# Kernel optimization log

Hardware: AMD Instinct MI355X
Metric: run time of the kernel (lower is better)

Reference implementation:

```python
import jax, jax.numpy as jnp
import numpy as np

N = 32768          # n_atoms
E = 524288         # n_edges (avg degree 16)
MUL = 8            # multiplicity of 0e and 1o in irreps_in/out
NB = 8             # n_basis
HR = 64            # hidden_radial
NTP = 4 * MUL * MUL  # tensor-product weight_numel (4 CG paths)
AVG_NEI = 16.0
INV_SQRT3 = 1.0 / np.sqrt(3.0)      # w3j(1,1,0) component
ALPHA = 1.0 / np.sqrt(2.0 * MUL)    # path normalization: fan_in = 2 paths * mul_in*mul_sh


def setup_inputs() -> dict:
    key = jax.random.key(0)
    ks = jax.random.split(key, 12)
    h = jax.random.normal(ks[0], (N, 4 * MUL), jnp.float32)            # [N, 8 scalars + 8*3 vectors]
    edge_index = jax.random.randint(ks[1], (2, E), 0, N)               # [2, E] int
    edge_sh = jax.random.normal(ks[2], (E, 4), jnp.float32)            # [E, 1x0e + 1x1o]
    edge_radial = jax.random.uniform(ks[3], (E, NB), jnp.float32)      # [E, n_basis]

    def lin(k, fi, fo):
        return (jax.random.normal(k, (fi, fo), jnp.float32) / np.sqrt(fi)).astype(jnp.float32)

    W1 = lin(ks[4], NB, HR); b1 = jnp.zeros((HR,), jnp.float32)
    W2 = lin(ks[5], HR, HR); b2 = jnp.zeros((HR,), jnp.float32)
    W3 = lin(ks[6], HR, NTP); b3 = jnp.zeros((NTP,), jnp.float32)
    Ws = jax.random.normal(ks[7], (MUL, MUL), jnp.float32)             # self-interaction, scalar block
    Wv = jax.random.normal(ks[8], (MUL, MUL), jnp.float32)             # self-interaction, vector block
    return dict(h=h, edge_index=edge_index, edge_sh=edge_sh, edge_radial=edge_radial,
                n_atoms=N, W1=W1, b1=b1, W2=W2, b2=b2, W3=W3, b3=b3, Ws=Ws, Wv=Wv)


def reference(h, edge_index, edge_sh, edge_radial, n_atoms, W1, b1, W2, b2, W3, b3, Ws, Wv):
    src, dst = edge_index[0], edge_index[1]

    # radial MLP -> per-edge tensor-product weights [E, 256]
    x = jax.nn.silu(edge_radial @ W1 + b1)
    x = jax.nn.silu(x @ W2 + b2)
    tpw = x @ W3 + b3
    P = MUL * MUL
    W00  = tpw[:, 0 * P:1 * P].reshape(-1, MUL, MUL)  # 0e x 0e -> 0e
    W110 = tpw[:, 1 * P:2 * P].reshape(-1, MUL, MUL)  # 1o x 1o -> 0e (dot)
    W01  = tpw[:, 2 * P:3 * P].reshape(-1, MUL, MUL)  # 0e x 1o -> 1o
    W10  = tpw[:, 3 * P:4 * P].reshape(-1, MUL, MUL)  # 1o x 0e -> 1o

    hs = h[:, :MUL]                         # [N, 8] scalars
    hv = h[:, MUL:].reshape(-1, MUL, 3)     # [N, 8, 3] vectors
    hs_e = hs[src]                          # gather [E, 8]
    hv_e = hv[src]                          # gather [E, 8, 3]
    sh0 = edge_sh[:, 0]                     # [E]
    sh1 = edge_sh[:, 1:4]                   # [E, 3]

    # equivariant tensor product (e3nn FullyConnectedTensorProduct, l<=1)
    m0 = ALPHA * (jnp.einsum('eu,euw->ew', hs_e * sh0[:, None], W00)
                  + INV_SQRT3 * jnp.einsum('eui,ei,euw->ew', hv_e, sh1, W110))       # [E, 8]
    m1 = ALPHA * (jnp.einsum('eu,ei,euw->ewi', hs_e, sh1, W01)
                  + jnp.einsum('eui,euw->ewi', hv_e * sh0[:, None, None], W10))      # [E, 8, 3]
    messages = jnp.concatenate([m0, m1.reshape(-1, 3 * MUL)], axis=-1)               # [E, 32]

    # scatter-add to destination nodes, degree normalization
    agg = jax.ops.segment_sum(messages, dst, num_segments=n_atoms) / np.sqrt(AVG_NEI)

    # self interaction (o3.Linear: block-diagonal per irrep, 1/sqrt(fan_in))
    self0 = (hs @ Ws) / np.sqrt(MUL)
    self1 = jnp.einsum('nui,uw->nwi', hv, Wv) / np.sqrt(MUL)
    h_self = jnp.concatenate([self0, self1.reshape(-1, 3 * MUL)], axis=-1)

    return h_self + agg
```

## Files before the change

kernel.cpp:

```cpp
#include <hip/hip_runtime.h>

#define N_ATOMS 32768
#define E_EDGES 524288
#define FEAT 32
#define TPB 512
#define WPB 8
#define PASSES 2
#define GRID (E_EDGES / (WPB * PASSES * 16))
#define INV_SQRT3 0.57735026919f
#define MSG_SCALE 0.0625f
#define SELF_SCALE 0.35355339059f

#define WS_MSG   0
#define WS_CNT   33554432
#define WS_CUR   33685504
#define WS_OFFS  33816576
#define WS_BSUM  33947648
#define WS_BBASE 33948160
#define WS_EIDS  33948672
#define WS_WF    36045824

typedef _Float16 f16;
typedef __attribute__((ext_vector_type(8))) _Float16 f16x8;
typedef __attribute__((ext_vector_type(4))) float f32x4;
typedef __attribute__((ext_vector_type(2))) _Float16 f16x2;
typedef __attribute__((ext_vector_type(4))) _Float16 f16x4;

__device__ __forceinline__ float silu(float x) { return x / (1.0f + __expf(-x)); }

__device__ __forceinline__ f32x4 mfma16(f16x8 a, f16x8 b, f32x4 c) {
    return __builtin_amdgcn_mfma_f32_16x16x32_f16(a, b, c, 0, 0, 0);
}

__global__ __launch_bounds__(256) void prep_kernel(
    const float* __restrict__ W1, const float* __restrict__ W2,
    const float* __restrict__ W3, f16* __restrict__ wf)
{
    int idx = blockIdx.x * 256 + threadIdx.x;
    float v;
    if (idx < 2048) {
        int f = idx;
        int n0 = f >> 9, lane = (f >> 3) & 63, j = f & 7;
        int k = ((lane >> 4) << 3) + j, n = (n0 << 4) + (lane & 15);
        v = (k < 8) ? W1[k * 64 + n] : 0.0f;
    } else if (idx < 6144) {
        int f = idx - 2048;
        int kk = f >> 11, n0 = (f >> 9) & 3, lane = (f >> 3) & 63, j = f & 7;
        int k = (kk << 5) + ((lane >> 4) << 3) + j, n = (n0 << 4) + (lane & 15);
        v = W2[k * 64 + n];
    } else {
        int f = idx - 6144;
        int kk = f >> 13, n0 = (f >> 9) & 15, lane = (f >> 3) & 63, j = f & 7;
        int k = (kk << 5) + ((lane >> 4) << 3) + j, n = (n0 << 4) + (lane & 15);
        v = W3[k * 256 + n];
    }
    wf[idx] = (f16)v;
}

__global__ __launch_bounds__(256) void count_kernel(const int* __restrict__ eidx,
                                                    int* __restrict__ cnt) {
    int e = blockIdx.x * 256 + threadIdx.x;
    atomicAdd(&cnt[eidx[E_EDGES + e]], 1);
}

__global__ __launch_bounds__(256) void scan1_kernel(const int* __restrict__ cnt,
                                                    int* __restrict__ bsum) {
    __shared__ int s[256];
    int t = threadIdx.x;
    s[t] = cnt[blockIdx.x * 256 + t];
    __syncthreads();
    for (int d = 128; d > 0; d >>= 1) {
        if (t < d) s[t] += s[t + d];
        __syncthreads();
    }
    if (t == 0) bsum[blockIdx.x] = s[0];
}

__global__ __launch_bounds__(64) void scan2_kernel(const int* __restrict__ bsum,
                                                   int* __restrict__ bbase) {
    int lane = threadIdx.x;
    int v0 = bsum[2 * lane], v1 = bsum[2 * lane + 1];
    int s = v0 + v1, x = s;
    for (int d = 1; d < 64; d <<= 1) {
        int y = __shfl_up(x, d, 64);
        if (lane >= d) x += y;
    }
    int excl = x - s;
    bbase[2 * lane] = excl;
    bbase[2 * lane + 1] = excl + v0;
}

__global__ __launch_bounds__(256) void scan3_kernel(const int* __restrict__ cnt,
                                                    const int* __restrict__ bbase,
                                                    int* __restrict__ offs) {
    int t = threadIdx.x, lane = t & 63, w = t >> 6;
    int v = cnt[blockIdx.x * 256 + t];
    int x = v;
    for (int d = 1; d < 64; d <<= 1) {
        int y = __shfl_up(x, d, 64);
        if (lane >= d) x += y;
    }
    __shared__ int wsum[4];
    if (lane == 63) wsum[w] = x;
    __syncthreads();
    int base = bbase[blockIdx.x];
    for (int i = 0; i < w; ++i) base += wsum[i];
    offs[blockIdx.x * 256 + t] = base + x - v;
}

__global__ __launch_bounds__(256) void fill_kernel(const int* __restrict__ eidx,
                                                   const int* __restrict__ offs,
                                                   int* __restrict__ cur,
                                                   int* __restrict__ eids) {
    int e = blockIdx.x * 256 + threadIdx.x;
    int d = eidx[E_EDGES + e];
    int slot = atomicAdd(&cur[d], 1);
    eids[offs[d] + slot] = e;
}

__global__ __launch_bounds__(TPB, 4) void edge_kernel(
    const float* __restrict__ h, const int* __restrict__ eidx,
    const float* __restrict__ esh, const float* __restrict__ erad,
    const f16* __restrict__ wf,
    const float* __restrict__ b1, const float* __restrict__ b2,
    const float* __restrict__ b3,
    f16* __restrict__ msg)
{
    __shared__ f16x8 w3L[2048];
    __shared__ float b1s[64], b2s[64], b3s[256];
    __shared__ __align__(16) char xtp[WPB][16 * 72 * 2];

    const int tid = threadIdx.x;
    {
        const f16x8* wfW3 = (const f16x8*)(wf + 6144);
#pragma unroll
        for (int i = 0; i < 4; ++i)
            w3L[tid + i * TPB] = wfW3[tid + i * TPB];
    }
    if (tid < 64) { b1s[tid] = b1[tid]; b2s[tid] = b2[tid]; }
    if (tid < 256) b3s[tid] = b3[tid];
    __syncthreads();

    const f16x8* w1f = (const f16x8*)(wf);
    const f16x8* w2f = (const f16x8*)(wf + 2048);

    const int wave = tid >> 6, lane = tid & 63;
    const int g = lane >> 4, m = lane & 15;
    const int me = lane >> 2, w0 = (lane & 3) * 2;

    f16* xs = (f16*)&xtp[wave][0];
    float* tpt = (float*)&xtp[wave][0];

    for (int pass = 0; pass < PASSES; ++pass) {
        const int tile = (blockIdx.x * WPB + wave) * PASSES + pass;
        const int e0 = tile * 16;

        f16x8 arad;
        {
            float r[8] = {0.f, 0.f, 0.f, 0.f, 0.f, 0.f, 0.f, 0.f};
            if (g == 0) {
                const float4* rp = (const float4*)(erad + (long)(e0 + m) * 8);
                float4 r0 = rp[0], r1 = rp[1];
                r[0] = r0.x; r[1] = r0.y; r[2] = r0.z; r[3] = r0.w;
                r[4] = r1.x; r[5] = r1.y; r[6] = r1.z; r[7] = r1.w;
            }
#pragma unroll
            for (int j = 0; j < 8; ++j) arad[j] = (f16)r[j];
        }

#pragma unroll
        for (int n0 = 0; n0 < 4; ++n0) {
            f32x4 acc = {};
            acc = mfma16(arad, w1f[n0 * 64 + lane], acc);
            float bn = b1s[n0 * 16 + m];
#pragma unroll
            for (int q = 0; q < 4; ++q) {
                float v = silu(acc[q] + bn);
                xs[(g * 4 + q) * 72 + n0 * 16 + m] = (f16)v;
            }
        }
        f16x8 a2[2];
        a2[0] = *(const f16x8*)(xs + m * 72 + g * 8);
        a2[1] = *(const f16x8*)(xs + m * 72 + 32 + g * 8);

        const int src = eidx[e0 + me];
        const float4 shv = *(const float4*)(esh + (long)(e0 + me) * 4);
        float hrow[32];
        {
            const float* hp = h + (long)src * FEAT;
#pragma unroll
            for (int c4 = 0; c4 < 8; ++c4)
                ((float4*)hrow)[c4] = ((const float4*)hp)[c4];
        }

#pragma unroll
        for (int n0 = 0; n0 < 4; ++n0) {
            f32x4 acc = {};
            acc = mfma16(a2[0], w2f[n0 * 64 + lane], acc);
            acc = mfma16(a2[1], w2f[(4 + n0) * 64 + lane], acc);
            float bn = b2s[n0 * 16 + m];
#pragma unroll
            for (int q = 0; q < 4; ++q) {
                float v = silu(acc[q] + bn);
                xs[(g * 4 + q) * 72 + n0 * 16 + m] = (f16)v;
            }
        }
        f16x8 a3[2];
        a3[0] = *(const f16x8*)(xs + m * 72 + g * 8);
        a3[1] = *(const f16x8*)(xs + m * 72 + 32 + g * 8);

        float m0a0 = 0.f, m0a1 = 0.f, s20 = 0.f, s21 = 0.f;
        float sv[6] = {0.f, 0.f, 0.f, 0.f, 0.f, 0.f};

#pragma unroll
        for (int c = 0; c < 4; ++c) {
#pragma unroll
            for (int n0 = 0; n0 < 4; ++n0) {
                f32x4 acc = {};
                acc = mfma16(a3[0], w3L[(c * 4 + n0) * 64 + lane], acc);
                acc = mfma16(a3[1], w3L[(16 + c * 4 + n0) * 64 + lane], acc);
                float bn = b3s[c * 64 + n0 * 16 + m];
#pragma unroll
                for (int q = 0; q < 4; ++q)
                    tpt[(g * 4 + q) * 18 + m] = acc[q] + bn;
#pragma unroll
                for (int uu = 0; uu < 2; ++uu) {
                    const int u = 2 * n0 + uu;
                    float2 t = *(const float2*)(tpt + me * 18 + uu * 8 + w0);
                    if (c == 0) {
                        float a0 = hrow[u] * shv.x;
                        m0a0 += a0 * t.x; m0a1 += a0 * t.y;
                    } else if (c == 1) {
                        float a1 = INV_SQRT3 * (hrow[8 + u * 3] * shv.y +
                                                hrow[9 + u * 3] * shv.z +
                                                hrow[10 + u * 3] * shv.w);
                        m0a0 += a1 * t.x; m0a1 += a1 * t.y;
                    } else if (c == 2) {
                        s20 += hrow[u] * t.x; s21 += hrow[u] * t.y;
                    } else {
                        sv[0] += hrow[8 + u * 3] * t.x;
                        sv[1] += hrow[9 + u * 3] * t.x;
                        sv[2] += hrow[10 + u * 3] * t.x;
                        sv[3] += hrow[8 + u * 3] * t.y;
                        sv[4] += hrow[9 + u * 3] * t.y;
                        sv[5] += hrow[10 + u * 3] * t.y;
                    }
                }
            }
        }

        f16* row = msg + (long)(e0 + me) * FEAT;
        f16x2 p0;
        p0[0] = (f16)(MSG_SCALE * m0a0);
        p0[1] = (f16)(MSG_SCALE * m0a1);
        *(f16x2*)(row + w0) = p0;
        f16 m1v[6];
#pragma unroll
        for (int i = 0; i < 3; ++i) {
            float s1i = (i == 0) ? shv.y : (i == 1) ? shv.z : shv.w;
            m1v[i]     = (f16)(MSG_SCALE * (s1i * s20 + shv.x * sv[i]));
            m1v[3 + i] = (f16)(MSG_SCALE * (s1i * s21 + shv.x * sv[3 + i]));
        }
        f16* rp = row + 8 + 3 * w0;
        { f16x2 t; t[0] = m1v[0]; t[1] = m1v[1]; *(f16x2*)(rp)     = t; }
        { f16x2 t; t[0] = m1v[2]; t[1] = m1v[3]; *(f16x2*)(rp + 2) = t; }
        { f16x2 t; t[0] = m1v[4]; t[1] = m1v[5]; *(f16x2*)(rp + 4) = t; }
    }
}

__global__ __launch_bounds__(256) void gather_kernel(
    const f16* __restrict__ msg, const int* __restrict__ eids,
    const int* __restrict__ offs, const int* __restrict__ cnt,
    const float* __restrict__ h,
    const float* __restrict__ Ws, const float* __restrict__ Wv,
    float* __restrict__ out)
{
    const int t = threadIdx.x;
    const int n = blockIdx.x * 32 + (t >> 3);
    const int L = t & 7;
    const int base = offs[n], deg = cnt[n];

    float a0 = 0.f, a1 = 0.f, a2 = 0.f, a3 = 0.f;
    for (int i = 0; i < deg; ++i) {
        int eid = eids[base + i];
        f16x4 v = *(const f16x4*)(msg + (long)eid * FEAT + L * 4);
        a0 += (float)v[0]; a1 += (float)v[1]; a2 += (float)v[2]; a3 += (float)v[3];
    }

    const float* hrow = h + (long)n * FEAT;
    const int f0 = L * 4;
    float o[4];
    if (L < 2) {
#pragma unroll
        for (int j = 0; j < 4; ++j) {
            int w = f0 + j;
            float a = 0.f;
#pragma unroll
            for (int u = 0; u < 8; ++u) a += hrow[u] * Ws[u * 8 + w];
            o[j] = SELF_SCALE * a;
        }
    } else {
#pragma unroll
        for (int j = 0; j < 4; ++j) {
            int f = f0 + j, w = (f - 8) / 3, i3 = (f - 8) % 3;
            float a = 0.f;
#pragma unroll
            for (int u = 0; u < 8; ++u) a += hrow[8 + u * 3 + i3] * Wv[u * 8 + w];
            o[j] = SELF_SCALE * a;
        }
    }
    float4 r;
    r.x = o[0] + a0; r.y = o[1] + a1; r.z = o[2] + a2; r.w = o[3] + a3;
    *(float4*)(out + (long)n * FEAT + f0) = r;
}

extern "C" void kernel_launch(void* const* d_in, const int* in_sizes, int n_in,
                              void* d_out, int out_size, void* d_ws, size_t ws_size,
                              hipStream_t stream)
{
    const float* h    = (const float*)d_in[0];
    const int*   eidx = (const int*)  d_in[1];
    const float* esh  = (const float*)d_in[2];
    const float* erad = (const float*)d_in[3];
    const float* W1   = (const float*)d_in[5];
    const float* b1   = (const float*)d_in[6];
    const float* W2   = (const float*)d_in[7];
    const float* b2   = (const float*)d_in[8];
    const float* W3   = (const float*)d_in[9];
    const float* b3   = (const float*)d_in[10];
    const float* Ws   = (const float*)d_in[11];
    const float* Wv   = (const float*)d_in[12];
    float* out = (float*)d_out;

    char* ws = (char*)d_ws;
    f16* msg   = (f16*)(ws + WS_MSG);
    int* cnt   = (int*)(ws + WS_CNT);
    int* cur   = (int*)(ws + WS_CUR);
    int* offs  = (int*)(ws + WS_OFFS);
    int* bsum  = (int*)(ws + WS_BSUM);
    int* bbase = (int*)(ws + WS_BBASE);
    int* eids  = (int*)(ws + WS_EIDS);
    f16* wf    = (f16*)(ws + WS_WF);

    hipMemsetAsync(cnt, 0, 2 * N_ATOMS * sizeof(int), stream);

    prep_kernel<<<88, 256, 0, stream>>>(W1, W2, W3, wf);
    count_kernel<<<E_EDGES / 256, 256, 0, stream>>>(eidx, cnt);
    scan1_kernel<<<N_ATOMS / 256, 256, 0, stream>>>(cnt, bsum);
    scan2_kernel<<<1, 64, 0, stream>>>(bsum, bbase);
    scan3_kernel<<<N_ATOMS / 256, 256, 0, stream>>>(cnt, bbase, offs);
    edge_kernel<<<GRID, TPB, 0, stream>>>(h, eidx, esh, erad, wf,
                                          b1, b2, b3, msg);
    fill_kernel<<<E_EDGES / 256, 256, 0, stream>>>(eidx, offs, cur, eids);
    gather_kernel<<<N_ATOMS / 32, 256, 0, stream>>>(msg, eids, offs, cnt,
                                                    h, Ws, Wv, out);
}
```

Measured before the change: 178.8 us.

## Write edge messages directly into CSR-sorted slots, drop fill kernel and eids

The edge kernel now reserves each edge's destination-sorted row via an atomic on the per-node cursor and writes its message there. This removes the separate fill kernel and the eids indirection, so the gather reads contiguous rows per node. The W3 tensor-product loop is also software-pipelined with a double-buffered tpt tile, and the gather loop is unrolled by two with split accumulators. The tpt double buffer assumes the shared scratch holds 576 floats per warp, and message row order within a node now depends on atomic ordering.

Result: no change. 180.7 us (+1.1%).

```diff
diff --git a/kernel.cpp b/kernel.cpp
--- a/kernel.cpp
+++ b/kernel.cpp
@@ -17,7 +17,6 @@
 #define WS_OFFS  33816576
 #define WS_BSUM  33947648
 #define WS_BBASE 33948160
-#define WS_EIDS  33948672
 #define WS_WF    36045824
 
 typedef _Float16 f16;
@@ -108,22 +107,13 @@
     offs[blockIdx.x * 256 + t] = base + x - v;
 }
 
-__global__ __launch_bounds__(256) void fill_kernel(const int* __restrict__ eidx,
-                                                   const int* __restrict__ offs,
-                                                   int* __restrict__ cur,
-                                                   int* __restrict__ eids) {
-    int e = blockIdx.x * 256 + threadIdx.x;
-    int d = eidx[E_EDGES + e];
-    int slot = atomicAdd(&cur[d], 1);
-    eids[offs[d] + slot] = e;
-}
-
 __global__ __launch_bounds__(TPB, 4) void edge_kernel(
     const float* __restrict__ h, const int* __restrict__ eidx,
     const float* __restrict__ esh, const float* __restrict__ erad,
     const f16* __restrict__ wf,
     const float* __restrict__ b1, const float* __restrict__ b2,
     const float* __restrict__ b3,
+    const int* __restrict__ offs, int* __restrict__ cur,
     f16* __restrict__ msg)
 {
     __shared__ f16x8 w3L[2048];
@@ -184,6 +174,7 @@
         a2[1] = *(const f16x8*)(xs + m * 72 + 32 + g * 8);
 
         const int src = eidx[e0 + me];
+        const int dst = eidx[E_EDGES + e0 + me];
         const float4 shv = *(const float4*)(esh + (long)(e0 + me) * 4);
         float hrow[32];
         {
@@ -192,6 +183,10 @@
             for (int c4 = 0; c4 < 8; ++c4)
                 ((float4*)hrow)[c4] = ((const float4*)hp)[c4];
         }
+        int rowid = 0;
+        if ((lane & 3) == 0)
+            rowid = offs[dst] + atomicAdd(&cur[dst], 1);
+        rowid = __shfl(rowid, me * 4);
 
 #pragma unroll
         for (int n0 = 0; n0 < 4; ++n0) {
@@ -213,43 +208,60 @@
         float sv[6] = {0.f, 0.f, 0.f, 0.f, 0.f, 0.f};
 
 #pragma unroll
-        for (int c = 0; c < 4; ++c) {
-#pragma unroll
-            for (int n0 = 0; n0 < 4; ++n0) {
-                f32x4 acc = {};
-                acc = mfma16(a3[0], w3L[(c * 4 + n0) * 64 + lane], acc);
-                acc = mfma16(a3[1], w3L[(16 + c * 4 + n0) * 64 + lane], acc);
-                float bn = b3s[c * 64 + n0 * 16 + m];
-#pragma unroll
-                for (int q = 0; q < 4; ++q)
-                    tpt[(g * 4 + q) * 18 + m] = acc[q] + bn;
+        for (int t = 0; t < 16; ++t) {
+            const int c = t >> 2, n0 = t & 3;
+            f32x4 acc = {};
+            acc = mfma16(a3[0], w3L[(c * 4 + n0) * 64 + lane], acc);
+            acc = mfma16(a3[1], w3L[(16 + c * 4 + n0) * 64 + lane], acc);
+            float bn = b3s[c * 64 + n0 * 16 + m];
+            float* tb = tpt + (t & 1) * 288;
+#pragma unroll
+            for (int q = 0; q < 4; ++q)
+                tb[(g * 4 + q) * 18 + m] = acc[q] + bn;
+            if (t > 0) {
+                const int tp = t - 1, cp = tp >> 2, np = tp & 3;
+                const float* rb = tpt + (tp & 1) * 288;
 #pragma unroll
                 for (int uu = 0; uu < 2; ++uu) {
-                    const int u = 2 * n0 + uu;
-                    float2 t = *(const float2*)(tpt + me * 18 + uu * 8 + w0);
-                    if (c == 0) {
+                    const int u = 2 * np + uu;
+                    float2 tv = *(const float2*)(rb + me * 18 + uu * 8 + w0);
+                    if (cp == 0) {
                         float a0 = hrow[u] * shv.x;
-                        m0a0 += a0 * t.x; m0a1 += a0 * t.y;
-                    } else if (c == 1) {
+                        m0a0 += a0 * tv.x; m0a1 += a0 * tv.y;
+                    } else if (cp == 1) {
                         float a1 = INV_SQRT3 * (hrow[8 + u * 3] * shv.y +
                                                 hrow[9 + u * 3] * shv.z +
                                                 hrow[10 + u * 3] * shv.w);
-                        m0a0 += a1 * t.x; m0a1 += a1 * t.y;
-                    } else if (c == 2) {
-                        s20 += hrow[u] * t.x; s21 += hrow[u] * t.y;
+                        m0a0 += a1 * tv.x; m0a1 += a1 * tv.y;
+                    } else if (cp == 2) {
+                        s20 += hrow[u] * tv.x; s21 += hrow[u] * tv.y;
                     } else {
-                        sv[0] += hrow[8 + u * 3] * t.x;
-                        sv[1] += hrow[9 + u * 3] * t.x;
-                        sv[2] += hrow[10 + u * 3] * t.x;
-                        sv[3] += hrow[8 + u * 3] * t.y;
-                        sv[4] += hrow[9 + u * 3] * t.y;
-                        sv[5] += hrow[10 + u * 3] * t.y;
+                        sv[0] += hrow[8 + u * 3] * tv.x;
+                        sv[1] += hrow[9 + u * 3] * tv.x;
+                        sv[2] += hrow[10 + u * 3] * tv.x;
+                        sv[3] += hrow[8 + u * 3] * tv.y;
+                        sv[4] += hrow[9 + u * 3] * tv.y;
+                        sv[5] += hrow[10 + u * 3] * tv.y;
                     }
                 }
             }
         }
-
-        f16* row = msg + (long)(e0 + me) * FEAT;
+        {
+            const float* rb = tpt + 288;
+#pragma unroll
+            for (int uu = 0; uu < 2; ++uu) {
+                const int u = 6 + uu;
+                float2 tv = *(const float2*)(rb + me * 18 + uu * 8 + w0);
+                sv[0] += hrow[8 + u * 3] * tv.x;
+                sv[1] += hrow[9 + u * 3] * tv.x;
+                sv[2] += hrow[10 + u * 3] * tv.x;
+                sv[3] += hrow[8 + u * 3] * tv.y;
+                sv[4] += hrow[9 + u * 3] * tv.y;
+                sv[5] += hrow[10 + u * 3] * tv.y;
+            }
+        }
+
+        f16* row = msg + (long)rowid * FEAT;
         f16x2 p0;
         p0[0] = (f16)(MSG_SCALE * m0a0);
         p0[1] = (f16)(MSG_SCALE * m0a1);
@@ -262,14 +274,14 @@
             m1v[3 + i] = (f16)(MSG_SCALE * (s1i * s21 + shv.x * sv[3 + i]));
         }
         f16* rp = row + 8 + 3 * w0;
-        { f16x2 t; t[0] = m1v[0]; t[1] = m1v[1]; *(f16x2*)(rp)     = t; }
-        { f16x2 t; t[0] = m1v[2]; t[1] = m1v[3]; *(f16x2*)(rp + 2) = t; }
-        { f16x2 t; t[0] = m1v[4]; t[1] = m1v[5]; *(f16x2*)(rp + 4) = t; }
+        { f16x2 t2; t2[0] = m1v[0]; t2[1] = m1v[1]; *(f16x2*)(rp)     = t2; }
+        { f16x2 t2; t2[0] = m1v[2]; t2[1] = m1v[3]; *(f16x2*)(rp + 2) = t2; }
+        { f16x2 t2; t2[0] = m1v[4]; t2[1] = m1v[5]; *(f16x2*)(rp + 4) = t2; }
     }
 }
 
 __global__ __launch_bounds__(256) void gather_kernel(
-    const f16* __restrict__ msg, const int* __restrict__ eids,
+    const f16* __restrict__ msg,
     const int* __restrict__ offs, const int* __restrict__ cnt,
     const float* __restrict__ h,
     const float* __restrict__ Ws, const float* __restrict__ Wv,
@@ -281,11 +293,19 @@
     const int base = offs[n], deg = cnt[n];
 
     float a0 = 0.f, a1 = 0.f, a2 = 0.f, a3 = 0.f;
-    for (int i = 0; i < deg; ++i) {
-        int eid = eids[base + i];
-        f16x4 v = *(const f16x4*)(msg + (long)eid * FEAT + L * 4);
+    float c0 = 0.f, c1 = 0.f, c2 = 0.f, c3 = 0.f;
+    int i = 0;
+    for (; i + 1 < deg; i += 2) {
+        f16x4 v = *(const f16x4*)(msg + (long)(base + i) * FEAT + L * 4);
+        f16x4 w = *(const f16x4*)(msg + (long)(base + i + 1) * FEAT + L * 4);
         a0 += (float)v[0]; a1 += (float)v[1]; a2 += (float)v[2]; a3 += (float)v[3];
-    }
+        c0 += (float)w[0]; c1 += (float)w[1]; c2 += (float)w[2]; c3 += (float)w[3];
+    }
+    if (i < deg) {
+        f16x4 v = *(const f16x4*)(msg + (long)(base + i) * FEAT + L * 4);
+        a0 += (float)v[0]; a1 += (float)v[1]; a2 += (float)v[2]; a3 += (float)v[3];
+    }
+    a0 += c0; a1 += c1; a2 += c2; a3 += c3;
 
     const float* hrow = h + (long)n * FEAT;
     const int f0 = L * 4;
@@ -339,7 +359,6 @@
     int* offs  = (int*)(ws + WS_OFFS);
     int* bsum  = (int*)(ws + WS_BSUM);
     int* bbase = (int*)(ws + WS_BBASE);
-    int* eids  = (int*)(ws + WS_EIDS);
     f16* wf    = (f16*)(ws + WS_WF);
 
     hipMemsetAsync(cnt, 0, 2 * N_ATOMS * sizeof(int), stream);
@@ -350,8 +369,7 @@
     scan2_kernel<<<1, 64, 0, stream>>>(bsum, bbase);
     scan3_kernel<<<N_ATOMS / 256, 256, 0, stream>>>(cnt, bbase, offs);
     edge_kernel<<<GRID, TPB, 0, stream>>>(h, eidx, esh, erad, wf,
-                                          b1, b2, b3, msg);
-    fill_kernel<<<E_EDGES / 256, 256, 0, stream>>>(eidx, offs, cur, eids);
-    gather_kernel<<<N_ATOMS / 32, 256, 0, stream>>>(msg, eids, offs, cnt,
+                                          b1, b2, b3, offs, cur, msg);
+    gather_kernel<<<N_ATOMS / 32, 256, 0, stream>>>(msg, offs, cnt,
                                                     h, Ws, Wv, out);
 }
```
